# Performance work log

Measured on AMD Instinct MI355X. Metric: run time of the kernel, lower is better.

The kernel has to match this reference:

```python
import jax, jax.numpy as jnp
import numpy as np

B, S, D, H = 32, 1024, 256, 256


def setup_inputs() -> dict:
    key = jax.random.key(0)
    ks = jax.random.split(key, 7)
    s_in = 1.0 / np.sqrt(D)
    s_h = 1.0 / np.sqrt(H)
    x = jax.random.normal(ks[0], (B, S, D), dtype=jnp.float32)
    # gate order: i, f, g, o stacked along last dim -> 4H
    W_fwd = jax.random.uniform(ks[1], (D, 4 * H), dtype=jnp.float32, minval=-s_in, maxval=s_in)
    U_fwd = jax.random.uniform(ks[2], (H, 4 * H), dtype=jnp.float32, minval=-s_h, maxval=s_h)
    b_fwd = jax.random.uniform(ks[3], (4 * H,), dtype=jnp.float32, minval=-s_in, maxval=s_in)
    W_rev = jax.random.uniform(ks[4], (D, 4 * H), dtype=jnp.float32, minval=-s_in, maxval=s_in)
    U_rev = jax.random.uniform(ks[5], (H, 4 * H), dtype=jnp.float32, minval=-s_h, maxval=s_h)
    b_rev = jax.random.uniform(ks[6], (4 * H,), dtype=jnp.float32, minval=-s_in, maxval=s_in)
    return {"x": x, "W_fwd": W_fwd, "U_fwd": U_fwd, "b_fwd": b_fwd,
            "W_rev": W_rev, "U_rev": U_rev, "b_rev": b_rev}


def _lstm_scan(x, W, U, b):
    # x: [B, S, D] -> outputs h over time: [B, S, H]
    hdim = U.shape[0]
    # precompute input projection for all steps: [S, B, 4H]
    xW = jnp.einsum('bsd,dg->sbg', x, W) + b

    def step(carry, xw_t):
        h, c = carry
        gates = xw_t + h @ U  # [B, 4H]
        i_t = jax.nn.sigmoid(gates[:, 0 * hdim:1 * hdim])
        f_t = jax.nn.sigmoid(gates[:, 1 * hdim:2 * hdim])
        g_t = jnp.tanh(gates[:, 2 * hdim:3 * hdim])
        o_t = jax.nn.sigmoid(gates[:, 3 * hdim:4 * hdim])
        c_t = f_t * c + i_t * g_t
        h_t = o_t * jnp.tanh(c_t)
        return (h_t, c_t), h_t

    bsz = x.shape[0]
    h0 = jnp.zeros((bsz, hdim), dtype=x.dtype)
    c0 = jnp.zeros((bsz, hdim), dtype=x.dtype)
    _, hs = jax.lax.scan(step, (h0, c0), xW)
    return jnp.transpose(hs, (1, 0, 2))  # [B, S, H]


def reference(x, W_fwd, U_fwd, b_fwd, W_rev, U_rev, b_rev):
    out_f = _lstm_scan(x, W_fwd, U_fwd, b_fwd)
    out_r = _lstm_scan(x[:, ::-1, :], W_rev, U_rev, b_rev)[:, ::-1, :]
    return jnp.concatenate([out_f, out_r], axis=2)  # [B, S, 2H]
```

## Files before the change

kernel.cpp:

```cpp
#include <hip/hip_runtime.h>
#include <hip/hip_bf16.h>

typedef _Float16 f16;
typedef _Float16 half8 __attribute__((ext_vector_type(8)));
typedef float f32x4 __attribute__((ext_vector_type(4)));
typedef int i32x4 __attribute__((ext_vector_type(4)));


__global__ void prep_uq_kernel(const float* __restrict__ Uf, const float* __restrict__ Ur,
                               unsigned int* __restrict__ UQm, float* __restrict__ Uscale)
{
    int idx = blockIdx.x * 256 + threadIdx.x;
    if (idx >= 2048) return;
    int dir = idx >> 10, c = idx & 1023;
    const float* U = dir ? Ur : Uf;
    float m = 0.f;
    for (int k = 0; k < 256; ++k) m = fmaxf(m, fabsf(U[k * 1024 + c]));
    float sinv = (m > 0.f) ? 127.f / m : 0.f;
    int tile = c >> 4, colr = c & 15;
    uint4* UQm4 = (uint4*)UQm;
    for (int ks = 0; ks < 4; ++ks) {
        #pragma unroll
        for (int kg = 0; kg < 4; ++kg) {
            unsigned int w[4];
            #pragma unroll
            for (int d = 0; d < 4; ++d) {
                unsigned int wd = 0;
                #pragma unroll
                for (int e = 0; e < 4; ++e) {
                    int k = ks * 64 + kg * 16 + d * 4 + e;
                    int q = __float2int_rn(U[k * 1024 + c] * sinv);
                    wd |= ((unsigned int)(q & 0xff)) << (8 * e);
                }
                w[d] = wd;
            }
            UQm4[((size_t)((dir * 64 + tile) * 4 + ks)) * 64 + kg * 16 + colr] =
                make_uint4(w[0], w[1], w[2], w[3]);
        }
    }
    Uscale[idx] = m / (127.f * 127.f);
}

__global__ __launch_bounds__(256) void proj_gemm_kernel(
    const float* __restrict__ x, const float* __restrict__ Wf, const float* __restrict__ Wr,
    const float* __restrict__ bfw, const float* __restrict__ brw, f16* __restrict__ G)
{
    const int nt = blockIdx.x;
    const int mt = blockIdx.y;
    const int m0 = mt * 128, n0 = nt * 128;
    const int dir = n0 >> 10, nin0 = n0 & 1023;
    const float* W   = dir ? Wr : Wf;
    const float* bia = dir ? brw : bfw;
    __shared__ f16 Asm[128][40];
    __shared__ f16 Bsm[128][40];
    const int t = threadIdx.x;
    const int lane = t & 63, wave = t >> 6;
    const int wr = wave >> 1, wc = wave & 1;
    f32x4 acc[4][4] = {};
    for (int k0 = 0; k0 < 256; k0 += 32) {
        #pragma unroll
        for (int e = 0; e < 16; ++e) {
            int idx = e * 256 + t;
            int r = idx >> 5, kk = idx & 31;
            Asm[r][kk] = (f16)x[(size_t)(m0 + r) * 256 + (k0 + kk)];
        }
        #pragma unroll
        for (int e = 0; e < 16; ++e) {
            int idx = e * 256 + t;
            int col = idx & 127, kr = idx >> 7;
            Bsm[col][kr] = (f16)W[(size_t)(k0 + kr) * 1024 + (nin0 + col)];
        }
        __syncthreads();
        const int l15 = lane & 15, kb = (lane >> 4) * 8;
        half8 af[4], bfr[4];
        #pragma unroll
        for (int fr = 0; fr < 4; ++fr) af[fr]  = *(const half8*)&Asm[wr * 64 + fr * 16 + l15][kb];
        #pragma unroll
        for (int fc = 0; fc < 4; ++fc) bfr[fc] = *(const half8*)&Bsm[wc * 64 + fc * 16 + l15][kb];
        #pragma unroll
        for (int fr = 0; fr < 4; ++fr)
            #pragma unroll
            for (int fc = 0; fc < 4; ++fc)
                acc[fr][fc] = __builtin_amdgcn_mfma_f32_16x16x32_f16(af[fr], bfr[fc], acc[fr][fc], 0, 0, 0);
        __syncthreads();
    }
    const int row4 = (lane >> 4) * 4, c15 = lane & 15;
    #pragma unroll
    for (int fr = 0; fr < 4; ++fr)
        #pragma unroll
        for (int fc = 0; fc < 4; ++fc) {
            int rbase = m0 + wr * 64 + fr * 16 + row4;
            int cidx  = n0 + wc * 64 + fc * 16 + c15;
            float bv = bia[cidx & 1023];
            #pragma unroll
            for (int i = 0; i < 4; ++i)
                G[(size_t)(rbase + i) * 2048 + cidx] = (f16)(acc[fr][fc][i] + bv);
        }
}

__device__ __forceinline__ float tanh_fast(float x) {
    float e = __expf(2.f * x);
    return 1.f - 2.f / (e + 1.f);
}

__global__
__attribute__((amdgpu_flat_work_group_size(1024, 1024)))
__attribute__((amdgpu_waves_per_eu(4, 4)))
void scan_kernel(
    const f16* __restrict__ G, const unsigned int* __restrict__ UQm,
    const float* __restrict__ Uscale, float* __restrict__ out)
{
    const int wg = blockIdx.x;
    const int dir = wg >> 5, b = wg & 31;
    const int tid = threadIdx.x;
    const int wave = tid >> 6, lane = tid & 63;
    const bool is_gate = (tid < 256);
    const int gc = tid & 255;

    __shared__ __align__(16) unsigned int hq[64];
    __shared__ float pre[1024];

    if (tid < 64) hq[tid] = 0u;

    const i32x4* UQm4 = (const i32x4*)UQm;
    i32x4 uf[4][4];
    #pragma unroll
    for (int tau = 0; tau < 4; ++tau)
        #pragma unroll
        for (int ks = 0; ks < 4; ++ks)
            uf[tau][ks] = UQm4[((size_t)((dir * 64 + wave * 4 + tau) * 4 + ks)) * 64 + lane];

    float usc[4] = {0.f, 0.f, 0.f, 0.f};
    if (lane < 16) {
        #pragma unroll
        for (int tau = 0; tau < 4; ++tau)
            usc[tau] = Uscale[dir * 1024 + wave * 64 + tau * 16 + lane];
    }

    const f16* Grow = G + (size_t)b * 1024 * 2048 + dir * 1024 + gc;
    float* outp = out + (size_t)b * 1024 * 512 + dir * 256 + gc;
    float xwc0 = 0.f, xwc1 = 0.f, xwc2 = 0.f, xwc3 = 0.f;
    float c_state = 0.f;
    const int s0 = dir ? 1023 : 0;
    if (is_gate) {
        xwc0 = (float)Grow[(size_t)s0 * 2048 + 0];
        xwc1 = (float)Grow[(size_t)s0 * 2048 + 256];
        xwc2 = (float)Grow[(size_t)s0 * 2048 + 512];
        xwc3 = (float)Grow[(size_t)s0 * 2048 + 768];
    }
    __syncthreads();

    const char* hqb = (const char*)hq;
    const int arow = (lane >> 4) << 4;

    for (int t = 0; t < 1024; ++t) {
        const int s  = dir ? (1023 - t) : t;
        const int tn = (t < 1023) ? (t + 1) : t;
        const int sn = dir ? (1023 - tn) : tn;

        f16 xn0, xn1, xn2, xn3;
        if (is_gate) {
            xn0 = Grow[(size_t)sn * 2048 + 0];
            xn1 = Grow[(size_t)sn * 2048 + 256];
            xn2 = Grow[(size_t)sn * 2048 + 512];
            xn3 = Grow[(size_t)sn * 2048 + 768];
        }

        i32x4 acc0 = {0,0,0,0}, acc1 = {0,0,0,0}, acc2 = {0,0,0,0}, acc3 = {0,0,0,0};
        #pragma unroll
        for (int ks = 0; ks < 4; ++ks) {
            i32x4 a = *(const i32x4*)(hqb + ks * 64 + arow);
            acc0 = __builtin_amdgcn_mfma_i32_16x16x64_i8(a, uf[0][ks], acc0, 0, 0, 0);
            acc1 = __builtin_amdgcn_mfma_i32_16x16x64_i8(a, uf[1][ks], acc1, 0, 0, 0);
            acc2 = __builtin_amdgcn_mfma_i32_16x16x64_i8(a, uf[2][ks], acc2, 0, 0, 0);
            acc3 = __builtin_amdgcn_mfma_i32_16x16x64_i8(a, uf[3][ks], acc3, 0, 0, 0);
        }
        if (lane < 16) {
            pre[wave * 64 +  0 + lane] = (float)acc0[0] * usc[0];
            pre[wave * 64 + 16 + lane] = (float)acc1[0] * usc[1];
            pre[wave * 64 + 32 + lane] = (float)acc2[0] * usc[2];
            pre[wave * 64 + 48 + lane] = (float)acc3[0] * usc[3];
        }
        __syncthreads();

        if (is_gate) {
            float pi = pre[gc      ] + xwc0;
            float pf = pre[gc + 256] + xwc1;
            float pg = pre[gc + 512] + xwc2;
            float po = pre[gc + 768] + xwc3;
            float ig = 1.f / (1.f + __expf(-pi));
            float fg = 1.f / (1.f + __expf(-pf));
            float gg = tanh_fast(pg);
            float og = 1.f / (1.f + __expf(-po));
            c_state = fg * c_state + ig * gg;
            float h = og * tanh_fast(c_state);
            outp[(size_t)s * 512] = h;
            ((signed char*)hq)[gc] = (signed char)__float2int_rn(h * 127.f);
            xwc0 = (float)xn0; xwc1 = (float)xn1; xwc2 = (float)xn2; xwc3 = (float)xn3;
        }
        __syncthreads();
    }
}

extern "C" void kernel_launch(void* const* d_in, const int* in_sizes, int n_in,
                              void* d_out, int out_size, void* d_ws, size_t ws_size,
                              hipStream_t stream) {
    const float* x  = (const float*)d_in[0];
    const float* Wf = (const float*)d_in[1];
    const float* Uf = (const float*)d_in[2];
    const float* bf = (const float*)d_in[3];
    const float* Wr = (const float*)d_in[4];
    const float* Ur = (const float*)d_in[5];
    const float* br = (const float*)d_in[6];
    float* out = (float*)d_out;

    char* ws = (char*)d_ws;
    unsigned int* UQm = (unsigned int*)ws;
    float* Uscale     = (float*)(ws + (size_t)512 * 1024);
    f16* G            = (f16*)(ws + (size_t)1024 * 1024);

    prep_uq_kernel<<<8, 256, 0, stream>>>(Uf, Ur, UQm, Uscale);
    dim3 gg(16, 256);
    proj_gemm_kernel<<<gg, 256, 0, stream>>>(x, Wf, Wr, bf, br, G);
    scan_kernel<<<64, 1024, 0, stream>>>(G, UQm, Uscale, out);
}
```

Before: 1.054 ms.

## Remap gate columns per wave and double-buffer h to drop a barrier

Each wave now computes the i, f, g and o gate columns for the same 16 hidden units, so the wave that produces the pre-activations also applies the LSTM epilogue in registers. This removes the shared-memory pre buffer and one of the two block-wide barriers per timestep. The quantized h vector is double-buffered so the next step's writes cannot race with the current step's reads. Only 16 lanes per wave do the epilogue, which spreads the pointwise work across all 16 waves instead of the first 4.

New measurement: 1.290 ms. 22.4% more time.

```diff
diff --git a/kernel.cpp b/kernel.cpp
--- a/kernel.cpp
+++ b/kernel.cpp
@@ -114,44 +114,45 @@
     const int dir = wg >> 5, b = wg & 31;
     const int tid = threadIdx.x;
     const int wave = tid >> 6, lane = tid & 63;
-    const bool is_gate = (tid < 256);
-    const int gc = tid & 255;
-
-    __shared__ __align__(16) unsigned int hq[64];
-    __shared__ float pre[1024];
-
+    const bool ep = (lane < 16);
+
+    __shared__ __align__(16) unsigned int hq[128];
     if (tid < 64) hq[tid] = 0u;
 
     const i32x4* UQm4 = (const i32x4*)UQm;
-    i32x4 uf[4][4];
+    i32x4 uf0[4], uf1[4], uf2[4], uf3[4];
     #pragma unroll
-    for (int tau = 0; tau < 4; ++tau)
-        #pragma unroll
-        for (int ks = 0; ks < 4; ++ks)
-            uf[tau][ks] = UQm4[((size_t)((dir * 64 + wave * 4 + tau) * 4 + ks)) * 64 + lane];
-
-    float usc[4] = {0.f, 0.f, 0.f, 0.f};
-    if (lane < 16) {
-        #pragma unroll
-        for (int tau = 0; tau < 4; ++tau)
-            usc[tau] = Uscale[dir * 1024 + wave * 64 + tau * 16 + lane];
-    }
-
-    const f16* Grow = G + (size_t)b * 1024 * 2048 + dir * 1024 + gc;
-    float* outp = out + (size_t)b * 1024 * 512 + dir * 256 + gc;
-    float xwc0 = 0.f, xwc1 = 0.f, xwc2 = 0.f, xwc3 = 0.f;
+    for (int ks = 0; ks < 4; ++ks) {
+        uf0[ks] = UQm4[((size_t)((dir * 64 + ( 0 + wave)) * 4 + ks)) * 64 + lane];
+        uf1[ks] = UQm4[((size_t)((dir * 64 + (16 + wave)) * 4 + ks)) * 64 + lane];
+        uf2[ks] = UQm4[((size_t)((dir * 64 + (32 + wave)) * 4 + ks)) * 64 + lane];
+        uf3[ks] = UQm4[((size_t)((dir * 64 + (48 + wave)) * 4 + ks)) * 64 + lane];
+    }
+
+    float usc0 = 0.f, usc1 = 0.f, usc2 = 0.f, usc3 = 0.f;
+    if (ep) {
+        usc0 = Uscale[dir * 1024 +   0 + wave * 16 + lane];
+        usc1 = Uscale[dir * 1024 + 256 + wave * 16 + lane];
+        usc2 = Uscale[dir * 1024 + 512 + wave * 16 + lane];
+        usc3 = Uscale[dir * 1024 + 768 + wave * 16 + lane];
+    }
+
+    const f16* Gg = G + (size_t)b * 1024 * 2048 + dir * 1024 + wave * 16 + lane;
+    float* outp = out + (size_t)b * 1024 * 512 + dir * 256 + wave * 16 + lane;
+    float xw0 = 0.f, xw1 = 0.f, xw2 = 0.f, xw3 = 0.f;
+    const int s0 = dir ? 1023 : 0;
+    if (ep) {
+        xw0 = (float)Gg[(size_t)s0 * 2048 +   0];
+        xw1 = (float)Gg[(size_t)s0 * 2048 + 256];
+        xw2 = (float)Gg[(size_t)s0 * 2048 + 512];
+        xw3 = (float)Gg[(size_t)s0 * 2048 + 768];
+    }
     float c_state = 0.f;
-    const int s0 = dir ? 1023 : 0;
-    if (is_gate) {
-        xwc0 = (float)Grow[(size_t)s0 * 2048 + 0];
-        xwc1 = (float)Grow[(size_t)s0 * 2048 + 256];
-        xwc2 = (float)Grow[(size_t)s0 * 2048 + 512];
-        xwc3 = (float)Grow[(size_t)s0 * 2048 + 768];
-    }
     __syncthreads();
 
-    const char* hqb = (const char*)hq;
+    char* hqb = (char*)hq;
     const int arow = (lane >> 4) << 4;
+    int p = 0;
 
     for (int t = 0; t < 1024; ++t) {
         const int s  = dir ? (1023 - t) : t;
@@ -159,35 +160,28 @@
         const int sn = dir ? (1023 - tn) : tn;
 
         f16 xn0, xn1, xn2, xn3;
-        if (is_gate) {
-            xn0 = Grow[(size_t)sn * 2048 + 0];
-            xn1 = Grow[(size_t)sn * 2048 + 256];
-            xn2 = Grow[(size_t)sn * 2048 + 512];
-            xn3 = Grow[(size_t)sn * 2048 + 768];
+        if (ep) {
+            xn0 = Gg[(size_t)sn * 2048 +   0];
+            xn1 = Gg[(size_t)sn * 2048 + 256];
+            xn2 = Gg[(size_t)sn * 2048 + 512];
+            xn3 = Gg[(size_t)sn * 2048 + 768];
         }
 
         i32x4 acc0 = {0,0,0,0}, acc1 = {0,0,0,0}, acc2 = {0,0,0,0}, acc3 = {0,0,0,0};
         #pragma unroll
         for (int ks = 0; ks < 4; ++ks) {
-            i32x4 a = *(const i32x4*)(hqb + ks * 64 + arow);
-            acc0 = __builtin_amdgcn_mfma_i32_16x16x64_i8(a, uf[0][ks], acc0, 0, 0, 0);
-            acc1 = __builtin_amdgcn_mfma_i32_16x16x64_i8(a, uf[1][ks], acc1, 0, 0, 0);
-            acc2 = __builtin_amdgcn_mfma_i32_16x16x64_i8(a, uf[2][ks], acc2, 0, 0, 0);
-            acc3 = __builtin_amdgcn_mfma_i32_16x16x64_i8(a, uf[3][ks], acc3, 0, 0, 0);
-        }
-        if (lane < 16) {
-            pre[wave * 64 +  0 + lane] = (float)acc0[0] * usc[0];
-            pre[wave * 64 + 16 + lane] = (float)acc1[0] * usc[1];
-            pre[wave * 64 + 32 + lane] = (float)acc2[0] * usc[2];
-            pre[wave * 64 + 48 + lane] = (float)acc3[0] * usc[3];
-        }
-        __syncthreads();
-
-        if (is_gate) {
-            float pi = pre[gc      ] + xwc0;
-            float pf = pre[gc + 256] + xwc1;
-            float pg = pre[gc + 512] + xwc2;
-            float po = pre[gc + 768] + xwc3;
+            i32x4 a = *(const i32x4*)(hqb + p * 256 + ks * 64 + arow);
+            acc0 = __builtin_amdgcn_mfma_i32_16x16x64_i8(a, uf0[ks], acc0, 0, 0, 0);
+            acc1 = __builtin_amdgcn_mfma_i32_16x16x64_i8(a, uf1[ks], acc1, 0, 0, 0);
+            acc2 = __builtin_amdgcn_mfma_i32_16x16x64_i8(a, uf2[ks], acc2, 0, 0, 0);
+            acc3 = __builtin_amdgcn_mfma_i32_16x16x64_i8(a, uf3[ks], acc3, 0, 0, 0);
+        }
+
+        if (ep) {
+            float pi = (float)acc0[0] * usc0 + xw0;
+            float pf = (float)acc1[0] * usc1 + xw1;
+            float pg = (float)acc2[0] * usc2 + xw2;
+            float po = (float)acc3[0] * usc3 + xw3;
             float ig = 1.f / (1.f + __expf(-pi));
             float fg = 1.f / (1.f + __expf(-pf));
             float gg = tanh_fast(pg);
@@ -195,10 +189,12 @@
             c_state = fg * c_state + ig * gg;
             float h = og * tanh_fast(c_state);
             outp[(size_t)s * 512] = h;
-            ((signed char*)hq)[gc] = (signed char)__float2int_rn(h * 127.f);
-            xwc0 = (float)xn0; xwc1 = (float)xn1; xwc2 = (float)xn2; xwc3 = (float)xn3;
+            hqb[(1 - p) * 256 + wave * 16 + lane] =
+                (char)(signed char)__float2int_rn(h * 127.f);
+            xw0 = (float)xn0; xw1 = (float)xn1; xw2 = (float)xn2; xw3 = (float)xn3;
         }
         __syncthreads();
+        p ^= 1;
     }
 }
 
```
